# Kernel optimization log

Measured on AMD Instinct MI355X. Metric: run time of the kernel, lower is better.

The kernel has to match this reference:

```python
import jax, jax.numpy as jnp
import numpy as np


def setup_inputs() -> dict:
    key = jax.random.key(0)
    ks = jax.random.split(key, 4)
    B, T, D, U = 64, 512, 1024, 1024
    scale = 1.0 / np.sqrt(D)
    return {
        "x": jax.random.normal(ks[0], (B, T, D), dtype=jnp.float32),
        "kernel_z": jax.random.normal(ks[1], (D, U), dtype=jnp.float32) * scale,
        "kernel_r": jax.random.normal(ks[2], (D, U), dtype=jnp.float32) * scale,
        "kernel_h": jax.random.normal(ks[3], (D, U), dtype=jnp.float32) * scale,
        "memory_z": jnp.ones((U,), dtype=jnp.float32),
        "memory_r": jnp.ones((U,), dtype=jnp.float32),
        "bias_z": jnp.zeros((U,), dtype=jnp.float32),
        "bias_r": jnp.zeros((U,), dtype=jnp.float32),
        "bias_h": jnp.zeros((U,), dtype=jnp.float32),
    }


def _bru_scan(x, kernel_z, kernel_r, kernel_h, memory_z, memory_r,
              bias_z, bias_r, bias_h):
    B, T, D = x.shape
    U = kernel_z.shape[1]
    # Precompute the three input projections for all timesteps at once
    # (same math as per-step K.dot; hoisted out of the recurrence).
    xz = jnp.einsum('btd,du->btu', x, kernel_z) + bias_z  # [B,T,U]
    xr = jnp.einsum('btd,du->btu', x, kernel_r) + bias_r
    xh = jnp.einsum('btd,du->btu', x, kernel_h) + bias_h

    def step(h, xs):
        xz_t, xr_t, xh_t = xs
        r = jnp.tanh(xr_t + h * memory_r) + 1.0
        z = jax.nn.sigmoid(xz_t + h * memory_z)
        hh = jnp.tanh(xh_t + r * h)
        out = (1.0 - z) * hh + z * h
        return out, out

    h0 = jnp.zeros((B, U), dtype=x.dtype)
    # scan over time axis
    xs = (jnp.swapaxes(xz, 0, 1), jnp.swapaxes(xr, 0, 1), jnp.swapaxes(xh, 0, 1))
    _, outs = jax.lax.scan(step, h0, xs)  # outs: [T,B,U]
    return jnp.swapaxes(outs, 0, 1)  # [B,T,U]


def reference(x, kernel_z, kernel_r, kernel_h, memory_z, memory_r,
              bias_z, bias_r, bias_h):
    return _bru_scan(x, kernel_z, kernel_r, kernel_h, memory_z, memory_r,
                     bias_z, bias_r, bias_h)
```

## Files before the change

### kernel.cpp

```cpp
#include <hip/hip_runtime.h>
#include <cmath>

using f16x8 = __attribute__((ext_vector_type(8))) _Float16;
using f32x4 = __attribute__((ext_vector_type(4))) float;

__device__ __forceinline__ void gld16(void* lds, const void* g) {
    __builtin_amdgcn_global_load_lds(
        (const __attribute__((address_space(1))) unsigned int*)g,
        (__attribute__((address_space(3))) unsigned int*)lds, 16, 0, 0);
}


__global__ __launch_bounds__(256)
void bru_conv_a(const float* __restrict__ x, char* __restrict__ Ablob,
                int T, int D, int Tc, int t0, int Mc)
{
    const int gid = blockIdx.x * 256 + threadIdx.x;
    const int kt = gid / Mc;
    const int m  = gid - kt * Mc;
    const int mt = m >> 8, row = m & 255;

    const long xrow = (long)(m / Tc) * T + t0 + (m % Tc);
    const float* src = x + xrow * (long)D + kt * 32;

    float v[32];
    #pragma unroll
    for (int i = 0; i < 8; ++i)
        *(float4*)&v[i * 4] = *(const float4*)(src + i * 4);

    _Float16 hi[32], lo[32];
    #pragma unroll
    for (int k = 0; k < 32; ++k) {
        hi[k] = (_Float16)v[k];
        lo[k] = (_Float16)(v[k] - (float)hi[k]);
    }

    char* base = Ablob + ((size_t)(mt * 32 + kt)) * 32768 + (size_t)row * 128;
    #pragma unroll
    for (int qe = 0; qe < 8; ++qe) {
        _Float16 o[8];
        #pragma unroll
        for (int j = 0; j < 8; ++j) {
            const int k = qe * 4 + (j >> 1);
            o[j] = (j & 1) ? lo[k] : hi[k];
        }
        *(f16x8*)(base + ((qe ^ (row & 7)) << 4)) = *(f16x8*)o;
    }
}

__global__ __launch_bounds__(256)
void bru_conv_w(const float* __restrict__ wz, const float* __restrict__ wr,
                const float* __restrict__ wh, char* __restrict__ Wblob,
                int D, int U)
{
    const int gid  = blockIdx.x * 256 + threadIdx.x;
    const int blob = gid >> 10;
    const int idx  = gid & 1023;
    const int row  = idx >> 3;
    const int s    = idx & 7;

    const int g    = blob >> 8;
    const int rest = blob & 255;
    const int nt   = rest >> 5;
    const int kt   = rest & 31;

    const float* W = (g == 0) ? wz : (g == 1) ? wr : wh;
    const int qe   = s ^ (row & 7);
    const int ucol = nt * 128 + row;

    _Float16 wf[4];
    #pragma unroll
    for (int jj = 0; jj < 4; ++jj)
        wf[jj] = (_Float16)W[(long)(kt * 32 + qe * 4 + jj) * U + ucol];

    _Float16 o[8];
    #pragma unroll
    for (int j = 0; j < 8; ++j) o[j] = wf[j >> 1];

    *(f16x8*)(Wblob + (size_t)blob * 16384 + (size_t)row * 128 + s * 16)
        = *(f16x8*)o;
}

__global__ __launch_bounds__(256, 2)
void bru_gemm_mfma(const char* __restrict__ Ablob, const char* __restrict__ Wblob,
                   const float* __restrict__ bz, const float* __restrict__ br,
                   const float* __restrict__ bh,
                   _Float16* __restrict__ proj,
                   int nmt, int U, int Mc)
{
    __shared__ char sm[49152];

    const int ngrid = gridDim.x;
    const int bid   = blockIdx.x;
    int lid = bid;
    if ((ngrid & 7) == 0) lid = (bid & 7) * (ngrid >> 3) + (bid >> 3);
    const int per_gate = nmt * 8;
    const int g  = lid / per_gate;
    const int r  = lid - g * per_gate;
    const int mt = r >> 3;
    const int nt = r & 7;

    const int tid    = threadIdx.x;
    const int lane   = tid & 63;
    const int w      = tid >> 6;
    const int wm     = w >> 1, wn = w & 1;
    const int lane15 = lane & 15;
    const int lgrp   = lane >> 4;
    const int r7     = lane15 & 7;

    const char* a_ptr = Ablob + (size_t)(mt * 32) * 32768 + tid * 16;
    const char* b_ptr = Wblob + (size_t)((g * 8 + nt) * 32) * 16384 + tid * 16;

    const int abase = (wm * 128 + lane15) * 128;
    const int bbase = 32768 + (wn * 64 + lane15) * 128;
    const int slot0 = ((lgrp    ) ^ r7) << 4;
    const int slot1 = ((lgrp + 4) ^ r7) << 4;

    f32x4 acc[8][4];
    #pragma unroll
    for (int i = 0; i < 8; ++i)
        #pragma unroll
        for (int j = 0; j < 4; ++j) acc[i][j] = (f32x4)0.f;

    for (int kt = 0; kt < 32; ++kt) {
        #pragma unroll
        for (int c = 0; c < 8; ++c)
            gld16(sm + c * 4096 + tid * 16, a_ptr + c * 4096);
        #pragma unroll
        for (int c = 0; c < 4; ++c)
            gld16(sm + 32768 + c * 4096 + tid * 16, b_ptr + c * 4096);
        a_ptr += 32768;
        b_ptr += 16384;
        __syncthreads();

        #pragma unroll
        for (int ks = 0; ks < 2; ++ks) {
            const int slot = ks ? slot1 : slot0;
            f16x8 af[8], bf[4];
            #pragma unroll
            for (int f = 0; f < 8; ++f)
                af[f] = *(const f16x8*)(sm + abase + f * 2048 + slot);
            #pragma unroll
            for (int j = 0; j < 4; ++j)
                bf[j] = *(const f16x8*)(sm + bbase + j * 2048 + slot);
            __builtin_amdgcn_s_setprio(1);
            #pragma unroll
            for (int f = 0; f < 8; ++f)
                #pragma unroll
                for (int j = 0; j < 4; ++j)
                    acc[f][j] = __builtin_amdgcn_mfma_f32_16x16x32_f16(
                        af[f], bf[j], acc[f][j], 0, 0, 0);
            __builtin_amdgcn_s_setprio(0);
        }
        __syncthreads();
    }

    const float* bias = (g == 0) ? bz : (g == 1) ? br : bh;
    const int n0 = nt * 128 + wn * 64;
    float bcol[4];
    #pragma unroll
    for (int j = 0; j < 4; ++j) bcol[j] = bias[n0 + j * 16 + lane15];

    _Float16* cbase = proj + (size_t)g * Mc * U + (size_t)n0 + lane15;
    #pragma unroll
    for (int f = 0; f < 8; ++f) {
        #pragma unroll
        for (int reg = 0; reg < 4; ++reg) {
            const int row = mt * 256 + wm * 128 + f * 16 + lgrp * 4 + reg;
            #pragma unroll
            for (int j = 0; j < 4; ++j)
                cbase[(size_t)row * U + j * 16] = (_Float16)(acc[f][j][reg] + bcol[j]);
        }
    }
}

#define PF 8
__global__ __launch_bounds__(256)
void bru_scan(const _Float16* __restrict__ proj,
              const float* __restrict__ mz, const float* __restrict__ mr,
              float* __restrict__ out,
              float* __restrict__ hstate,
              int B, int T, int U, int Tc, int t0, int Mc)
{
    const int idx = blockIdx.x * blockDim.x + threadIdx.x;
    const int b = idx / U;
    const int u = idx - b * U;

    float h = (t0 == 0) ? 0.f : hstate[idx];
    const float vmz = mz[u];
    const float vmr = mr[u];

    const _Float16* pz = proj + (long)b * Tc * U + u;
    const _Float16* pr = pz + (long)Mc * U;
    const _Float16* ph = pr + (long)Mc * U;
    float* po = out + ((long)b * T + t0) * U + u;

    _Float16 fz[PF], fr[PF], fh[PF];
    #pragma unroll
    for (int i = 0; i < PF; ++i) {
        const long o = (long)((i < Tc) ? i : (Tc - 1)) * U;
        fz[i] = pz[o]; fr[i] = pr[o]; fh[i] = ph[o];
    }

    for (int t = 0; t < Tc; t += PF) {
        #pragma unroll
        for (int i = 0; i < PF; ++i) {
            const float xz = (float)fz[i];
            const float xr = (float)fr[i];
            const float xh = (float)fh[i];
            {
                int tn = t + i + PF; if (tn > Tc - 1) tn = Tc - 1;
                const long o = (long)tn * U;
                fz[i] = pz[o]; fr[i] = pr[o]; fh[i] = ph[o];
            }
            const float e2r = __expf(2.f * (xr + h * vmr));
            const float rr  = 2.f - 2.f / (e2r + 1.f);
            const float zz  = 1.f / (1.f + __expf(-(xz + h * vmz)));
            const float e2h = __expf(2.f * (xh + rr * h));
            const float hh  = 1.f - 2.f / (e2h + 1.f);
            h = (1.f - zz) * hh + zz * h;
            if (t + i < Tc) po[(long)(t + i) * U] = h;
        }
    }
    hstate[idx] = h;
}

extern "C" void kernel_launch(void* const* d_in, const int* in_sizes, int n_in,
                              void* d_out, int out_size, void* d_ws, size_t ws_size,
                              hipStream_t stream)
{
    const float* x  = (const float*)d_in[0];
    const float* wz = (const float*)d_in[1];
    const float* wr = (const float*)d_in[2];
    const float* wh = (const float*)d_in[3];
    const float* mz = (const float*)d_in[4];
    const float* mr = (const float*)d_in[5];
    const float* bz = (const float*)d_in[6];
    const float* br = (const float*)d_in[7];
    const float* bh = (const float*)d_in[8];

    const int B = 64, T = 512, D = 1024, U = 1024;

    const size_t h_bytes = (size_t)B * U * sizeof(float);
    const size_t w_bytes = (size_t)768 * 16384;

    int Tc = T;
    while (Tc > 4) {
        const int Mc_ = B * Tc;
        const size_t a_bytes_ = (size_t)Mc_ * 4096;
        const size_t p_bytes_ = 3ull * Mc_ * U * sizeof(_Float16);
        if (h_bytes + w_bytes + a_bytes_ + p_bytes_ <= ws_size) break;
        Tc >>= 1;
    }
    const int nmt = B * Tc / 256;
    const int Mc  = B * Tc;
    const size_t a_bytes = (size_t)Mc * 4096;

    float*    h_state = (float*)d_ws;
    char*     Wblob   = (char*)d_ws + h_bytes;
    char*     Ablob   = (char*)d_ws + h_bytes + w_bytes;
    _Float16* proj    = (_Float16*)((char*)d_ws + h_bytes + w_bytes + a_bytes);

    bru_conv_w<<<768 * 1024 / 256, 256, 0, stream>>>(wz, wr, wh, Wblob, D, U);

    for (int t0 = 0; t0 < T; t0 += Tc) {
        bru_conv_a<<<(Mc * 32) / 256, 256, 0, stream>>>(x, Ablob, T, D, Tc, t0, Mc);

        bru_gemm_mfma<<<3 * nmt * 8, 256, 0, stream>>>(
            Ablob, Wblob, bz, br, bh, proj, nmt, U, Mc);

        bru_scan<<<(B * U) / 256, 256, 0, stream>>>(
            proj, mz, mr, (float*)d_out, h_state, B, T, U, Tc, t0, Mc);
    }
}
```

Baseline: 581.6 us.

## Triple-buffer GEMM pipeline with 256x256 tiles and split hi/lo A layout

```diff
diff --git a/kernel.cpp b/kernel.cpp
--- a/kernel.cpp
+++ b/kernel.cpp
@@ -35,16 +35,14 @@
         lo[k] = (_Float16)(v[k] - (float)hi[k]);
     }
 
-    char* base = Ablob + ((size_t)(mt * 32 + kt)) * 32768 + (size_t)row * 128;
-    #pragma unroll
-    for (int qe = 0; qe < 8; ++qe) {
-        _Float16 o[8];
-        #pragma unroll
-        for (int j = 0; j < 8; ++j) {
-            const int k = qe * 4 + (j >> 1);
-            o[j] = (j & 1) ? lo[k] : hi[k];
-        }
-        *(f16x8*)(base + ((qe ^ (row & 7)) << 4)) = *(f16x8*)o;
+    char* base = Ablob + ((size_t)(mt * 34 + kt)) * 32768 + (size_t)row * 128;
+    #pragma unroll
+    for (int q = 0; q < 4; ++q) {
+        _Float16 oh[8], ol[8];
+        #pragma unroll
+        for (int j = 0; j < 8; ++j) { oh[j] = hi[q * 8 + j]; ol[j] = lo[q * 8 + j]; }
+        *(f16x8*)(base + (((q    ) ^ (row & 7)) << 4)) = *(f16x8*)oh;
+        *(f16x8*)(base + (((q + 4) ^ (row & 7)) << 4)) = *(f16x8*)ol;
     }
 }
 
@@ -54,67 +52,61 @@
                 int D, int U)
 {
     const int gid  = blockIdx.x * 256 + threadIdx.x;
-    const int blob = gid >> 10;
-    const int idx  = gid & 1023;
-    const int row  = idx >> 3;
-    const int s    = idx & 7;
-
-    const int g    = blob >> 8;
-    const int rest = blob & 255;
+    const int blob = gid >> 8;
+    const int row  = gid & 255;
+
+    const int g    = blob >> 7;
+    const int rest = blob & 127;
     const int nt   = rest >> 5;
     const int kt   = rest & 31;
 
     const float* W = (g == 0) ? wz : (g == 1) ? wr : wh;
-    const int qe   = s ^ (row & 7);
-    const int ucol = nt * 128 + row;
-
-    _Float16 wf[4];
-    #pragma unroll
-    for (int jj = 0; jj < 4; ++jj)
-        wf[jj] = (_Float16)W[(long)(kt * 32 + qe * 4 + jj) * U + ucol];
-
-    _Float16 o[8];
-    #pragma unroll
-    for (int j = 0; j < 8; ++j) o[j] = wf[j >> 1];
-
-    *(f16x8*)(Wblob + (size_t)blob * 16384 + (size_t)row * 128 + s * 16)
-        = *(f16x8*)o;
-}
-
-__global__ __launch_bounds__(256, 2)
+    const int ucol = nt * 256 + row;
+
+    char* base = Wblob + ((size_t)((g * 4 + nt) * 34 + kt)) * 16384 + (size_t)row * 64;
+    #pragma unroll
+    for (int q = 0; q < 4; ++q) {
+        _Float16 o[8];
+        #pragma unroll
+        for (int j = 0; j < 8; ++j)
+            o[j] = (_Float16)W[(long)(kt * 32 + q * 8 + j) * U + ucol];
+        *(f16x8*)(base + ((q ^ ((row >> 1) & 3)) << 4)) = *(f16x8*)o;
+    }
+}
+
+__global__ __launch_bounds__(512, 2)
 void bru_gemm_mfma(const char* __restrict__ Ablob, const char* __restrict__ Wblob,
                    const float* __restrict__ bz, const float* __restrict__ br,
                    const float* __restrict__ bh,
                    _Float16* __restrict__ proj,
                    int nmt, int U, int Mc)
 {
-    __shared__ char sm[49152];
+    __shared__ char sm[147456];
 
     const int ngrid = gridDim.x;
     const int bid   = blockIdx.x;
     int lid = bid;
     if ((ngrid & 7) == 0) lid = (bid & 7) * (ngrid >> 3) + (bid >> 3);
-    const int per_gate = nmt * 8;
-    const int g  = lid / per_gate;
-    const int r  = lid - g * per_gate;
-    const int mt = r >> 3;
-    const int nt = r & 7;
-
-    const int tid    = threadIdx.x;
-    const int lane   = tid & 63;
-    const int w      = tid >> 6;
-    const int wm     = w >> 1, wn = w & 1;
-    const int lane15 = lane & 15;
-    const int lgrp   = lane >> 4;
-    const int r7     = lane15 & 7;
-
-    const char* a_ptr = Ablob + (size_t)(mt * 32) * 32768 + tid * 16;
-    const char* b_ptr = Wblob + (size_t)((g * 8 + nt) * 32) * 16384 + tid * 16;
-
-    const int abase = (wm * 128 + lane15) * 128;
-    const int bbase = 32768 + (wn * 64 + lane15) * 128;
-    const int slot0 = ((lgrp    ) ^ r7) << 4;
-    const int slot1 = ((lgrp + 4) ^ r7) << 4;
+    const int mt  = lid / 12;
+    const int rem = lid - mt * 12;
+    const int g   = rem >> 2;
+    const int nt  = rem & 3;
+
+    const int tid  = threadIdx.x;
+    const int lane = tid & 63;
+    const int w    = tid >> 6;
+    const int wm   = w >> 2, wn = w & 3;
+    const int l15  = lane & 15;
+    const int lgrp = lane >> 4;
+
+    const char* asrc = Ablob + (size_t)(mt * 34) * 32768;
+    const char* bsrc = Wblob + (size_t)((g * 4 + nt) * 34) * 16384;
+    const int st = tid * 16;
+
+    const int abase = (wm * 128 + l15) * 128;
+    const int slotA = (lgrp ^ (l15 & 7)) << 4;
+    const int bbase = 98304 + (wn * 64 + l15) * 64;
+    const int slotB = (lgrp ^ ((l15 >> 1) & 3)) << 4;
 
     f32x4 acc[8][4];
     #pragma unroll
@@ -122,46 +114,64 @@
         #pragma unroll
         for (int j = 0; j < 4; ++j) acc[i][j] = (f32x4)0.f;
 
+#define STAGE(kt_) do { \
+    const int bb_ = (kt_) % 3; \
+    _Pragma("unroll") for (int c_ = 0; c_ < 4; ++c_) \
+        gld16(sm + bb_ * 32768 + c_ * 8192 + st, \
+              asrc + (size_t)(kt_) * 32768 + c_ * 8192 + st); \
+    _Pragma("unroll") for (int c_ = 0; c_ < 2; ++c_) \
+        gld16(sm + 98304 + bb_ * 16384 + c_ * 8192 + st, \
+              bsrc + (size_t)(kt_) * 16384 + c_ * 8192 + st); } while (0)
+
+    STAGE(0); STAGE(1);
+    __builtin_amdgcn_sched_barrier(0);
+    asm volatile("s_waitcnt vmcnt(6)" ::: "memory");
+    __builtin_amdgcn_sched_barrier(0);
+    __builtin_amdgcn_s_barrier();
+
     for (int kt = 0; kt < 32; ++kt) {
-        #pragma unroll
-        for (int c = 0; c < 8; ++c)
-            gld16(sm + c * 4096 + tid * 16, a_ptr + c * 4096);
-        #pragma unroll
-        for (int c = 0; c < 4; ++c)
-            gld16(sm + 32768 + c * 4096 + tid * 16, b_ptr + c * 4096);
-        a_ptr += 32768;
-        b_ptr += 16384;
-        __syncthreads();
-
-        #pragma unroll
-        for (int ks = 0; ks < 2; ++ks) {
-            const int slot = ks ? slot1 : slot0;
-            f16x8 af[8], bf[4];
+        const int cb = kt % 3;
+
+        STAGE(kt + 2);
+
+        const char* sa = sm + cb * 32768;
+        const char* sb = sm + cb * 16384;
+        f16x8 ah[8], al[8], bf[4];
+        #pragma unroll
+        for (int f = 0; f < 8; ++f) {
+            ah[f] = *(const f16x8*)(sa + abase + f * 2048 + slotA);
+            al[f] = *(const f16x8*)(sa + abase + f * 2048 + (slotA ^ 64));
+        }
+        #pragma unroll
+        for (int j = 0; j < 4; ++j)
+            bf[j] = *(const f16x8*)(sb + bbase + j * 1024 + slotB);
+
+        asm volatile("s_waitcnt lgkmcnt(0)" ::: "memory");
+        __builtin_amdgcn_sched_barrier(0);
+        __builtin_amdgcn_s_setprio(1);
+        #pragma unroll
+        for (int f = 0; f < 8; ++f)
             #pragma unroll
-            for (int f = 0; f < 8; ++f)
-                af[f] = *(const f16x8*)(sm + abase + f * 2048 + slot);
-            #pragma unroll
-            for (int j = 0; j < 4; ++j)
-                bf[j] = *(const f16x8*)(sm + bbase + j * 2048 + slot);
-            __builtin_amdgcn_s_setprio(1);
-            #pragma unroll
-            for (int f = 0; f < 8; ++f)
-                #pragma unroll
-                for (int j = 0; j < 4; ++j)
-                    acc[f][j] = __builtin_amdgcn_mfma_f32_16x16x32_f16(
-                        af[f], bf[j], acc[f][j], 0, 0, 0);
-            __builtin_amdgcn_s_setprio(0);
-        }
-        __syncthreads();
-    }
+            for (int j = 0; j < 4; ++j) {
+                acc[f][j] = __builtin_amdgcn_mfma_f32_16x16x32_f16(ah[f], bf[j], acc[f][j], 0, 0, 0);
+                acc[f][j] = __builtin_amdgcn_mfma_f32_16x16x32_f16(al[f], bf[j], acc[f][j], 0, 0, 0);
+            }
+        __builtin_amdgcn_s_setprio(0);
+
+        __builtin_amdgcn_sched_barrier(0);
+        asm volatile("s_waitcnt vmcnt(6)" ::: "memory");
+        __builtin_amdgcn_sched_barrier(0);
+        __builtin_amdgcn_s_barrier();
+    }
+#undef STAGE
 
     const float* bias = (g == 0) ? bz : (g == 1) ? br : bh;
-    const int n0 = nt * 128 + wn * 64;
+    const int n0 = nt * 256 + wn * 64;
     float bcol[4];
     #pragma unroll
-    for (int j = 0; j < 4; ++j) bcol[j] = bias[n0 + j * 16 + lane15];
-
-    _Float16* cbase = proj + (size_t)g * Mc * U + (size_t)n0 + lane15;
+    for (int j = 0; j < 4; ++j) bcol[j] = bias[n0 + j * 16 + l15];
+
+    _Float16* cbase = proj + (size_t)g * Mc * U + (size_t)n0 + l15;
     #pragma unroll
     for (int f = 0; f < 8; ++f) {
         #pragma unroll
@@ -242,31 +252,31 @@
     const int B = 64, T = 512, D = 1024, U = 1024;
 
     const size_t h_bytes = (size_t)B * U * sizeof(float);
-    const size_t w_bytes = (size_t)768 * 16384;
+    const size_t w_bytes = (size_t)12 * 34 * 16384;
 
     int Tc = T;
     while (Tc > 4) {
-        const int Mc_ = B * Tc;
-        const size_t a_bytes_ = (size_t)Mc_ * 4096;
-        const size_t p_bytes_ = 3ull * Mc_ * U * sizeof(_Float16);
+        const int nmt_ = B * Tc / 256;
+        const size_t a_bytes_ = (size_t)nmt_ * 34 * 32768;
+        const size_t p_bytes_ = 3ull * B * Tc * U * sizeof(_Float16);
         if (h_bytes + w_bytes + a_bytes_ + p_bytes_ <= ws_size) break;
         Tc >>= 1;
     }
     const int nmt = B * Tc / 256;
     const int Mc  = B * Tc;
-    const size_t a_bytes = (size_t)Mc * 4096;
+    const size_t a_bytes = (size_t)nmt * 34 * 32768;
 
     float*    h_state = (float*)d_ws;
     char*     Wblob   = (char*)d_ws + h_bytes;
     char*     Ablob   = (char*)d_ws + h_bytes + w_bytes;
     _Float16* proj    = (_Float16*)((char*)d_ws + h_bytes + w_bytes + a_bytes);
 
-    bru_conv_w<<<768 * 1024 / 256, 256, 0, stream>>>(wz, wr, wh, Wblob, D, U);
+    bru_conv_w<<<12 * 32 * 256 / 256, 256, 0, stream>>>(wz, wr, wh, Wblob, D, U);
 
     for (int t0 = 0; t0 < T; t0 += Tc) {
         bru_conv_a<<<(Mc * 32) / 256, 256, 0, stream>>>(x, Ablob, T, D, Tc, t0, Mc);
 
-        bru_gemm_mfma<<<3 * nmt * 8, 256, 0, stream>>>(
+        bru_gemm_mfma<<<3 * nmt * 4, 512, 0, stream>>>(
             Ablob, Wblob, bz, br, bh, proj, nmt, U, Mc);
 
         bru_scan<<<(B * U) / 256, 256, 0, stream>>>(
```

New measurement: 554.8 us. 4.6% less time.
